# Kernel tuning notes

Hardware: AMD Instinct MI355X
Metric: run time of the kernel (lower is better)

The kernel has to match this reference:

```python
import math
import jax, jax.numpy as jnp
import numpy as np

NUM_BUCKETS = 32
MAX_DISTANCE = 128
N_HEADS = 16
D_KV = 64


def _relative_position_bucket(relative_position, num_buckets=NUM_BUCKETS, max_distance=MAX_DISTANCE):
    # bidirectional (encoder) version, faithful to T5Attention._relative_position_bucket
    nb = num_buckets // 2
    rel_buckets = (relative_position > 0).astype(jnp.int32) * nb
    rp = jnp.abs(relative_position)
    max_exact = nb // 2
    is_small = rp < max_exact
    # log-spaced buckets for large distances; clamp arg of log to >=1 to avoid -inf
    rp_large = max_exact + (
        jnp.log(jnp.maximum(rp, 1).astype(jnp.float32) / max_exact)
        / math.log(max_distance / max_exact)
        * (nb - max_exact)
    ).astype(jnp.int32)
    rp_large = jnp.minimum(rp_large, nb - 1)
    return rel_buckets + jnp.where(is_small, rp, rp_large)


def setup_inputs() -> dict:
    key = jax.random.key(0)
    ks = jax.random.split(key, 6)
    B, S, D = 2, 2048, 1024
    scale = 0.02
    return {
        "hidden_states": jax.random.normal(ks[0], (B, S, D), dtype=jnp.float32),
        "Wq": jax.random.normal(ks[1], (D, N_HEADS * D_KV), dtype=jnp.float32) * scale,
        "Wk": jax.random.normal(ks[2], (D, N_HEADS * D_KV), dtype=jnp.float32) * scale,
        "Wv": jax.random.normal(ks[3], (D, N_HEADS * D_KV), dtype=jnp.float32) * scale,
        "Wo": jax.random.normal(ks[4], (N_HEADS * D_KV, D), dtype=jnp.float32) * scale,
        "rel_bias": jax.random.normal(ks[5], (NUM_BUCKETS, N_HEADS), dtype=jnp.float32),
    }


def reference(hidden_states, Wq, Wk, Wv, Wo, rel_bias):
    B, S, D = hidden_states.shape
    H, dk = N_HEADS, D_KV
    q = (hidden_states @ Wq).reshape(B, S, H, dk)
    k = (hidden_states @ Wk).reshape(B, S, H, dk)
    v = (hidden_states @ Wv).reshape(B, S, H, dk)

    pos = jnp.arange(S)
    relative_position = pos[None, :] - pos[:, None]          # [S_q, S_k]
    buckets = _relative_position_bucket(relative_position)    # [S_q, S_k]
    bias = rel_bias[buckets].transpose(2, 0, 1)               # [H, S_q, S_k]

    # T5 attention: NO 1/sqrt(d) scaling
    scores = jnp.einsum('bqhd,bkhd->bhqk', q, k) + bias[None]
    attn = jax.nn.softmax(scores, axis=-1)
    ctx = jnp.einsum('bhqk,bkhd->bqhd', attn, v).reshape(B, S, H * dk)
    return ctx @ Wo
```

## Files before the change

### kernel.cpp

```cpp
#include <hip/hip_runtime.h>
#include <stdint.h>

#define S_LEN 2048
#define NH 16
#define NB_DELTA (2*S_LEN-1)
#define PST 72

typedef __attribute__((ext_vector_type(8))) __bf16 bf16x8;
typedef __attribute__((ext_vector_type(4))) float f32x4;

__device__ __forceinline__ unsigned short f2bf(float f){
    union { float f; unsigned int u; } v; v.f = f;
    unsigned int u = v.u;
    return (unsigned short)((u + 0x7FFFu + ((u >> 16) & 1u)) >> 16);
}
__device__ __forceinline__ unsigned short f2bf_fast(float f){
    union { float f; unsigned int u; } v; v.f = f;
    return (unsigned short)((v.u + 0x8000u) >> 16);
}
__device__ __forceinline__ float bf2f(unsigned short u){
    union { unsigned int u; float f; } v; v.u = ((unsigned int)u) << 16;
    return v.f;
}

__device__ __forceinline__ void gload16(const void* g, void* l){
    __builtin_amdgcn_global_load_lds(
        (const __attribute__((address_space(1))) void*)(uintptr_t)g,
        (__attribute__((address_space(3))) void*)(uintptr_t)l, 16, 0, 0);
}

__global__ __launch_bounds__(256) void prep_kernel(
    const float* __restrict__ hs, unsigned short* __restrict__ hsb,
    const float* __restrict__ W0, const float* __restrict__ W1,
    const float* __restrict__ W2, const float* __restrict__ W3,
    unsigned short* __restrict__ D0, unsigned short* __restrict__ D1,
    unsigned short* __restrict__ D2, unsigned short* __restrict__ D3,
    const float* __restrict__ rel_bias, float* __restrict__ biasT){
    if (blockIdx.z == 4) {
        int bi = blockIdx.y * 32 + blockIdx.x;
        for (int it = 0; it < 4; it++) {
            int i = bi * 4096 + it * 1024 + threadIdx.x * 4;
            float4 f = *(const float4*)(hs + i);
            ushort4 o;
            o.x = f2bf(f.x); o.y = f2bf(f.y); o.z = f2bf(f.z); o.w = f2bf(f.w);
            *(ushort4*)(hsb + i) = o;
        }
        if (bi < 16) {
            int t = bi * 256 + threadIdx.x;
            if (t < NB_DELTA) {
                int delta = t - (S_LEN - 1);
                int bucket = (delta > 0) ? 16 : 0;
                int a = delta < 0 ? -delta : delta;
                int b;
                if (a < 8) b = a;
                else {
                    int bl = 33 - __builtin_clz(a * a);
                    b = bl < 15 ? bl : 15;
                }
                bucket += b;
                for (int h = 0; h < NH; h++)
                    biasT[h * NB_DELTA + t] = rel_bias[bucket * NH + h];
            }
        }
        return;
    }
    const float* src; unsigned short* dst;
    switch (blockIdx.z) {
        case 0: src = W0; dst = D0; break;
        case 1: src = W1; dst = D1; break;
        case 2: src = W2; dst = D2; break;
        default: src = W3; dst = D3; break;
    }
    __shared__ float tile[32][33];
    int bx = blockIdx.x, by = blockIdx.y;
    int tx = threadIdx.x & 31, ty = threadIdx.x >> 5;
    for (int i = 0; i < 4; i++)
        tile[ty + 8*i][tx] = src[(size_t)(by*32 + ty + 8*i) * 1024 + bx*32 + tx];
    __syncthreads();
    for (int i = 0; i < 4; i++)
        dst[(size_t)(bx*32 + ty + 8*i) * 1024 + by*32 + tx] = f2bf(tile[tx][ty + 8*i]);
}

template<int MODE, int BM>
__global__ __launch_bounds__(256) void gemm_bt_kernel(const unsigned short* __restrict__ A,
                                                      const unsigned short* __restrict__ BT,
                                                      float* __restrict__ C0,
                                                      unsigned short* __restrict__ C1,
                                                      unsigned short* __restrict__ C2,
                                                      int Kdim, int ldc){
    constexpr int IT = BM / 32;
    __shared__ __align__(16) unsigned short As[BM * 32];
    __shared__ __align__(16) unsigned short Bs[128 * 32];
    const int t = threadIdx.x;
    const int wave = t >> 6, lane = t & 63;
    const int quad = lane >> 4, l16 = lane & 15;
    const int wm = (wave >> 1) * (BM / 2), wn = (wave & 1) * 64;
    const size_t row0 = (size_t)blockIdx.y * BM, col0 = (size_t)blockIdx.x * 128;

    const unsigned short* ga = A  + (row0 + wave * (BM/4) + (lane >> 2)) * (size_t)Kdim + (lane & 3) * 8;
    const unsigned short* gb = BT + (col0 + wave * 32 + (lane >> 2)) * (size_t)Kdim + (lane & 3) * 8;
    unsigned short* la0 = &As[(wave * (BM/4)) * 32];
    unsigned short* la1 = &As[(wave * (BM/4) + 16) * 32];
    unsigned short* lb0 = &Bs[(wave * 32) * 32];
    unsigned short* lb1 = &Bs[(wave * 32 + 16) * 32];
    const size_t rstep = (size_t)16 * Kdim;

    f32x4 acc[IT][4] = {};

    for (int kt = 0; kt < Kdim; kt += 32) {
        gload16(ga + kt, la0);
        if (BM == 128) gload16(ga + rstep + kt, la1);
        gload16(gb + kt,         lb0);
        gload16(gb + rstep + kt, lb1);
        __syncthreads();
        bf16x8 a[IT], b[4];
        for (int i = 0; i < IT; i++)
            a[i] = *(const bf16x8*)(&As[(wm + i*16 + l16) * 32 + quad * 8]);
        for (int j = 0; j < 4; j++)
            b[j] = *(const bf16x8*)(&Bs[(wn + j*16 + l16) * 32 + quad * 8]);
        for (int i = 0; i < IT; i++)
            for (int j = 0; j < 4; j++)
                acc[i][j] = __builtin_amdgcn_mfma_f32_16x16x32_bf16(a[i], b[j], acc[i][j], 0, 0, 0);
        __syncthreads();
    }
    for (int i = 0; i < IT; i++)
        for (int j = 0; j < 4; j++) {
            size_t r0 = row0 + wm + i*16 + quad*4;
            size_t c  = col0 + wn + j*16 + l16;
            if (MODE == 0) {
                for (int r = 0; r < 4; r++)
                    C0[(r0 + r) * ldc + c] = acc[i][j][r];
            } else {
                if (c < 2048) {
                    for (int r = 0; r < 4; r++)
                        C1[(r0 + r) * 2048 + c] = f2bf(acc[i][j][r]);
                } else {
                    int bb = (int)(r0 >> 11);
                    int s  = (int)(r0 & 2047);
                    ushort4 pk;
                    pk.x = f2bf(acc[i][j][0]); pk.y = f2bf(acc[i][j][1]);
                    pk.z = f2bf(acc[i][j][2]); pk.w = f2bf(acc[i][j][3]);
                    *(ushort4*)(C2 + ((size_t)(bb * 1024) + (c - 2048)) * 2048 + s) = pk;
                }
            }
        }
}

__global__ __launch_bounds__(256, 4) void flash6_kernel(
    const unsigned short* __restrict__ qk,
    const unsigned short* __restrict__ vt,
    const float* __restrict__ biasT,
    unsigned short* __restrict__ ctxpb,
    float* __restrict__ rsbuf)
{
    const int qt = blockIdx.x, h = blockIdx.y;
    const int b = blockIdx.z >> 1, ck = blockIdx.z & 1;
    const int kt0 = ck << 10;
    const int t = threadIdx.x;
    const int w = t >> 6, lane = t & 63, quad = lane >> 4, l16 = lane & 15;
    const int q0 = qt * 128;

    __shared__ __align__(16) unsigned short KV[4][64 * 32];
    __shared__ __align__(16) unsigned short Pb[128 * PST];
    __shared__ float bias_s[192];

    for (int s = 0; s < 4; s++) {
        int g = t + s * 256;
        int r = g >> 3, c = (g & 7) * 8;
        *(int4*)&Pb[r * PST + c] =
            *(const int4*)(qk + (size_t)(b * S_LEN + q0 + r) * 2048 + h * 64 + c);
    }
    __syncthreads();
    bf16x8 qb[2][2];
    for (int nt = 0; nt < 2; nt++)
        for (int ks = 0; ks < 2; ks++)
            qb[ks][nt] = *(const bf16x8*)&Pb[(w * 32 + nt * 16 + l16) * PST + ks * 32 + quad * 8];

    float rsum[2] = {0.f, 0.f};
    f32x4 ctx[4][2] = {};

    const float* biasRow = biasT + h * NB_DELTA + 2047;

    const int srow = w * 16 + (lane >> 2);
    const int scol = (lane & 3) * 8;
    unsigned short* ldsK0 = &KV[0][w * 16 * 32];
    unsigned short* ldsK1 = &KV[1][w * 16 * 32];
    unsigned short* ldsV0 = &KV[2][w * 16 * 32];
    unsigned short* ldsV1 = &KV[3][w * 16 * 32];

    for (int kt = kt0; kt < kt0 + 1024; kt += 64) {
        __syncthreads();
        {
            const unsigned short* kb = qk + (size_t)(b * S_LEN + kt + srow) * 2048 + 1024 + h * 64 + scol;
            const unsigned short* vb = vt + (size_t)(b * 1024 + h * 64 + srow) * 2048 + kt + scol;
            gload16(kb,      ldsK0);
            gload16(kb + 32, ldsK1);
            gload16(vb,      ldsV0);
            gload16(vb + 32, ldsV1);
            if (t < 192) bias_s[t] = biasRow[kt - q0 - 127 + t] - 16.0f;
        }
        __syncthreads();

        f32x4 st[4][2] = {};
        for (int ks = 0; ks < 2; ks++)
            for (int nb = 0; nb < 4; nb++) {
                bf16x8 ka = *(const bf16x8*)&KV[ks][(nb * 16 + l16) * 32 + quad * 8];
                st[nb][0] = __builtin_amdgcn_mfma_f32_16x16x32_bf16(ka, qb[ks][0], st[nb][0], 0, 0, 0);
                st[nb][1] = __builtin_amdgcn_mfma_f32_16x16x32_bf16(ka, qb[ks][1], st[nb][1], 0, 0, 0);
            }
        for (int nt = 0; nt < 2; nt++) {
            const int ib = quad * 4 + 127 - w * 32 - nt * 16 - l16;
            float rs = 0.f;
            for (int nb = 0; nb < 4; nb++) {
                float e0 = __expf(st[nb][nt][0] + bias_s[ib + nb * 16 + 0]);
                float e1 = __expf(st[nb][nt][1] + bias_s[ib + nb * 16 + 1]);
                float e2 = __expf(st[nb][nt][2] + bias_s[ib + nb * 16 + 2]);
                float e3 = __expf(st[nb][nt][3] + bias_s[ib + nb * 16 + 3]);
                rs += (e0 + e1) + (e2 + e3);
                ushort4 pk;
                pk.x = f2bf_fast(e0); pk.y = f2bf_fast(e1);
                pk.z = f2bf_fast(e2); pk.w = f2bf_fast(e3);
                *(ushort4*)&Pb[(w * 32 + nt * 16 + l16) * PST + nb * 16 + quad * 4] = pk;
            }
            rsum[nt] += rs;
        }
        for (int ks = 0; ks < 2; ks++) {
            bf16x8 pb0 = *(const bf16x8*)&Pb[(w * 32 + l16) * PST + ks * 32 + quad * 8];
            bf16x8 pb1 = *(const bf16x8*)&Pb[(w * 32 + 16 + l16) * PST + ks * 32 + quad * 8];
            for (int nd = 0; nd < 4; nd++) {
                bf16x8 va = *(const bf16x8*)&KV[2 + ks][(nd * 16 + l16) * 32 + quad * 8];
                ctx[nd][0] = __builtin_amdgcn_mfma_f32_16x16x32_bf16(va, pb0, ctx[nd][0], 0, 0, 0);
                ctx[nd][1] = __builtin_amdgcn_mfma_f32_16x16x32_bf16(va, pb1, ctx[nd][1], 0, 0, 0);
            }
        }
    }
    unsigned short* cp = ctxpb + (size_t)ck * 4096 * 1024;
    for (int nt = 0; nt < 2; nt++) {
        float rs = rsum[nt];
        rs += __shfl_xor(rs, 16, 64);
        rs += __shfl_xor(rs, 32, 64);
        int row = b * S_LEN + q0 + w * 32 + nt * 16 + l16;
        if (quad == 0) rsbuf[((size_t)ck * 4096 + row) * 16 + h] = rs;
        for (int nd = 0; nd < 4; nd++) {
            ushort4 pk;
            pk.x = f2bf(ctx[nd][nt][0]); pk.y = f2bf(ctx[nd][nt][1]);
            pk.z = f2bf(ctx[nd][nt][2]); pk.w = f2bf(ctx[nd][nt][3]);
            *(ushort4*)&cp[(size_t)row * 1024 + h * 64 + nd * 16 + quad * 4] = pk;
        }
    }
}

__global__ __launch_bounds__(256) void combine_kernel(const unsigned short* __restrict__ ctxpb,
                                                      const float* __restrict__ rsbuf,
                                                      unsigned short* __restrict__ ctxb){
    int e = blockIdx.x * 256 + threadIdx.x;
    int row = e >> 8;
    int c4 = (e & 255) * 4;
    int h = c4 >> 6;
    float l = rsbuf[(size_t)row * 16 + h] + rsbuf[((size_t)4096 + row) * 16 + h];
    ushort4 a  = *(const ushort4*)&ctxpb[(size_t)row * 1024 + c4];
    ushort4 b2 = *(const ushort4*)&ctxpb[(size_t)4096 * 1024 + (size_t)row * 1024 + c4];
    float inv = 1.f / l;
    ushort4 o;
    o.x = f2bf((bf2f(a.x) + bf2f(b2.x)) * inv);
    o.y = f2bf((bf2f(a.y) + bf2f(b2.y)) * inv);
    o.z = f2bf((bf2f(a.z) + bf2f(b2.z)) * inv);
    o.w = f2bf((bf2f(a.w) + bf2f(b2.w)) * inv);
    *(ushort4*)&ctxb[(size_t)row * 1024 + c4] = o;
}

extern "C" void kernel_launch(void* const* d_in, const int* in_sizes, int n_in,
                              void* d_out, int out_size, void* d_ws, size_t ws_size,
                              hipStream_t stream) {
    const float* hs       = (const float*)d_in[0];
    const float* Wq       = (const float*)d_in[1];
    const float* Wk       = (const float*)d_in[2];
    const float* Wv       = (const float*)d_in[3];
    const float* Wo       = (const float*)d_in[4];
    const float* rel_bias = (const float*)d_in[5];
    float* out = (float*)d_out;

    char* ws = (char*)d_ws;
    float* biasT          = (float*)ws;           ws += 262144;
    unsigned short* hsb   = (unsigned short*)ws;  ws += 8388608;
    unsigned short* WT    = (unsigned short*)ws;  ws += 6291456;
    unsigned short* WoT   = (unsigned short*)ws;  ws += 2097152;
    unsigned short* qkbuf = (unsigned short*)ws;  ws += 16777216;
    unsigned short* Vtg   = (unsigned short*)ws;  ws += 8388608;
    unsigned short* ctxb  = (unsigned short*)ws;  ws += 8388608;
    unsigned short* ctxpb = (unsigned short*)ws;  ws += 16777216;
    float* rsbuf          = (float*)ws;

    prep_kernel<<<dim3(32, 32, 5), 256, 0, stream>>>(
        hs, hsb, Wq, Wk, Wv, Wo,
        WT, WT + 1024 * 1024, WT + 2 * 1024 * 1024, WoT, rel_bias, biasT);

    gemm_bt_kernel<1, 128><<<dim3(24, 32), 256, 0, stream>>>(hsb, WT, nullptr, qkbuf, Vtg, 1024, 0);
    flash6_kernel<<<dim3(S_LEN / 128, NH, 4), 256, 0, stream>>>(qkbuf, Vtg, biasT, ctxpb, rsbuf);
    combine_kernel<<<4096, 256, 0, stream>>>(ctxpb, rsbuf, ctxb);
    gemm_bt_kernel<0, 64><<<dim3(8, 64), 256, 0, stream>>>(ctxb, WoT, out, nullptr, nullptr, 1024, 1024);
}
```

Before: 209.0 us.

## Swizzle LDS tiles with K=64 steps and move V transpose to separate kernel

The GEMM now stages 64-wide K tiles in shared memory with an XOR swizzle, which halves the number of loop iterations and barriers and is meant to avoid LDS bank conflicts. The QKV projection writes a plain row-major [tokens, 3072] buffer instead of a transposed V with strided ushort4 stores, and a new vtrans kernel produces the V^T layout. The flash kernel loads K and V into XOR-swizzled 64x64 LDS tiles. The cost is one extra kernel launch and an extra pass over V through global memory.

New measurement: 207.6 us. Within noise of the previous version (-0.7%).

```diff
diff --git a/kernel.cpp b/kernel.cpp
--- a/kernel.cpp
+++ b/kernel.cpp
@@ -86,41 +86,40 @@
                                                       const unsigned short* __restrict__ BT,
                                                       float* __restrict__ C0,
                                                       unsigned short* __restrict__ C1,
-                                                      unsigned short* __restrict__ C2,
                                                       int Kdim, int ldc){
     constexpr int IT = BM / 32;
-    __shared__ __align__(16) unsigned short As[BM * 32];
-    __shared__ __align__(16) unsigned short Bs[128 * 32];
+    __shared__ __align__(16) unsigned short As[BM * 64];
+    __shared__ __align__(16) unsigned short Bs[128 * 64];
     const int t = threadIdx.x;
     const int wave = t >> 6, lane = t & 63;
     const int quad = lane >> 4, l16 = lane & 15;
     const int wm = (wave >> 1) * (BM / 2), wn = (wave & 1) * 64;
     const size_t row0 = (size_t)blockIdx.y * BM, col0 = (size_t)blockIdx.x * 128;
 
-    const unsigned short* ga = A  + (row0 + wave * (BM/4) + (lane >> 2)) * (size_t)Kdim + (lane & 3) * 8;
-    const unsigned short* gb = BT + (col0 + wave * 32 + (lane >> 2)) * (size_t)Kdim + (lane & 3) * 8;
-    unsigned short* la0 = &As[(wave * (BM/4)) * 32];
-    unsigned short* la1 = &As[(wave * (BM/4) + 16) * 32];
-    unsigned short* lb0 = &Bs[(wave * 32) * 32];
-    unsigned short* lb1 = &Bs[(wave * 32 + 16) * 32];
-    const size_t rstep = (size_t)16 * Kdim;
+    const int srow8 = lane >> 3;
+    const int gg = (lane & 7) ^ srow8;
+    const unsigned short* gA = A  + (row0 + wave * 8 + srow8) * (size_t)Kdim + gg * 8;
+    const unsigned short* gB = BT + (col0 + wave * 8 + srow8) * (size_t)Kdim + gg * 8;
 
     f32x4 acc[IT][4] = {};
 
-    for (int kt = 0; kt < Kdim; kt += 32) {
-        gload16(ga + kt, la0);
-        if (BM == 128) gload16(ga + rstep + kt, la1);
-        gload16(gb + kt,         lb0);
-        gload16(gb + rstep + kt, lb1);
+    for (int kt = 0; kt < Kdim; kt += 64) {
+        for (int p = 0; p < BM / 32; p++)
+            gload16(gA + (size_t)(p * 32) * Kdim + kt, &As[(p * 32 + wave * 8) * 64]);
+        for (int p = 0; p < 4; p++)
+            gload16(gB + (size_t)(p * 32) * Kdim + kt, &Bs[(p * 32 + wave * 8) * 64]);
         __syncthreads();
-        bf16x8 a[IT], b[4];
-        for (int i = 0; i < IT; i++)
-            a[i] = *(const bf16x8*)(&As[(wm + i*16 + l16) * 32 + quad * 8]);
-        for (int j = 0; j < 4; j++)
-            b[j] = *(const bf16x8*)(&Bs[(wn + j*16 + l16) * 32 + quad * 8]);
-        for (int i = 0; i < IT; i++)
+        bf16x8 a[2][IT], b[2][4];
+        for (int ks = 0; ks < 2; ks++) {
+            for (int i = 0; i < IT; i++)
+                a[ks][i] = *(const bf16x8*)(&As[(wm + i*16 + l16) * 64 + (((ks*4 + quad) ^ (l16 & 7)) * 8)]);
             for (int j = 0; j < 4; j++)
-                acc[i][j] = __builtin_amdgcn_mfma_f32_16x16x32_bf16(a[i], b[j], acc[i][j], 0, 0, 0);
+                b[ks][j] = *(const bf16x8*)(&Bs[(wn + j*16 + l16) * 64 + (((ks*4 + quad) ^ (l16 & 7)) * 8)]);
+        }
+        for (int ks = 0; ks < 2; ks++)
+            for (int i = 0; i < IT; i++)
+                for (int j = 0; j < 4; j++)
+                    acc[i][j] = __builtin_amdgcn_mfma_f32_16x16x32_bf16(a[ks][i], b[ks][j], acc[i][j], 0, 0, 0);
         __syncthreads();
     }
     for (int i = 0; i < IT; i++)
@@ -131,23 +130,34 @@
                 for (int r = 0; r < 4; r++)
                     C0[(r0 + r) * ldc + c] = acc[i][j][r];
             } else {
-                if (c < 2048) {
-                    for (int r = 0; r < 4; r++)
-                        C1[(r0 + r) * 2048 + c] = f2bf(acc[i][j][r]);
-                } else {
-                    int bb = (int)(r0 >> 11);
-                    int s  = (int)(r0 & 2047);
-                    ushort4 pk;
-                    pk.x = f2bf(acc[i][j][0]); pk.y = f2bf(acc[i][j][1]);
-                    pk.z = f2bf(acc[i][j][2]); pk.w = f2bf(acc[i][j][3]);
-                    *(ushort4*)(C2 + ((size_t)(bb * 1024) + (c - 2048)) * 2048 + s) = pk;
-                }
-            }
-        }
-}
-
-__global__ __launch_bounds__(256, 4) void flash6_kernel(
-    const unsigned short* __restrict__ qk,
+                for (int r = 0; r < 4; r++)
+                    C1[(r0 + r) * ldc + c] = f2bf(acc[i][j][r]);
+            }
+        }
+}
+
+__global__ __launch_bounds__(256) void vtrans_kernel(const unsigned short* __restrict__ qkv,
+                                                     unsigned short* __restrict__ vt){
+    __shared__ unsigned short tile[64][72];
+    const int v0 = blockIdx.x * 64, s0 = blockIdx.y * 64, b = blockIdx.z;
+    const int tx = threadIdx.x & 7, ty = threadIdx.x >> 3;
+    for (int i = 0; i < 2; i++)
+        *(int4*)&tile[ty + 32*i][tx * 8] =
+            *(const int4*)(qkv + (size_t)(b * 2048 + s0 + ty + 32*i) * 3072 + 2048 + v0 + tx * 8);
+    __syncthreads();
+    for (int i = 0; i < 2; i++) {
+        int v = ty + 32*i;
+        int sl = tx * 8;
+        ushort4 o0, o1;
+        o0.x = tile[sl+0][v]; o0.y = tile[sl+1][v]; o0.z = tile[sl+2][v]; o0.w = tile[sl+3][v];
+        o1.x = tile[sl+4][v]; o1.y = tile[sl+5][v]; o1.z = tile[sl+6][v]; o1.w = tile[sl+7][v];
+        unsigned short* dst = vt + (size_t)(b * 1024 + v0 + v) * 2048 + s0 + sl;
+        *(ushort4*)dst = o0; *(ushort4*)(dst + 4) = o1;
+    }
+}
+
+__global__ __launch_bounds__(256, 4) void flash7_kernel(
+    const unsigned short* __restrict__ qkv,
     const unsigned short* __restrict__ vt,
     const float* __restrict__ biasT,
     unsigned short* __restrict__ ctxpb,
@@ -160,7 +170,8 @@
     const int w = t >> 6, lane = t & 63, quad = lane >> 4, l16 = lane & 15;
     const int q0 = qt * 128;
 
-    __shared__ __align__(16) unsigned short KV[4][64 * 32];
+    __shared__ __align__(16) unsigned short Ks[64 * 64];
+    __shared__ __align__(16) unsigned short Vs[64 * 64];
     __shared__ __align__(16) unsigned short Pb[128 * PST];
     __shared__ float bias_s[192];
 
@@ -168,7 +179,7 @@
         int g = t + s * 256;
         int r = g >> 3, c = (g & 7) * 8;
         *(int4*)&Pb[r * PST + c] =
-            *(const int4*)(qk + (size_t)(b * S_LEN + q0 + r) * 2048 + h * 64 + c);
+            *(const int4*)(qkv + (size_t)(b * S_LEN + q0 + r) * 3072 + h * 64 + c);
     }
     __syncthreads();
     bf16x8 qb[2][2];
@@ -181,22 +192,19 @@
 
     const float* biasRow = biasT + h * NB_DELTA + 2047;
 
-    const int srow = w * 16 + (lane >> 2);
-    const int scol = (lane & 3) * 8;
-    unsigned short* ldsK0 = &KV[0][w * 16 * 32];
-    unsigned short* ldsK1 = &KV[1][w * 16 * 32];
-    unsigned short* ldsV0 = &KV[2][w * 16 * 32];
-    unsigned short* ldsV1 = &KV[3][w * 16 * 32];
+    const int srow8 = lane >> 3;
+    const int gg = (lane & 7) ^ srow8;
+    const int swz = ((l16 & 7) * 8);
 
     for (int kt = kt0; kt < kt0 + 1024; kt += 64) {
         __syncthreads();
         {
-            const unsigned short* kb = qk + (size_t)(b * S_LEN + kt + srow) * 2048 + 1024 + h * 64 + scol;
-            const unsigned short* vb = vt + (size_t)(b * 1024 + h * 64 + srow) * 2048 + kt + scol;
-            gload16(kb,      ldsK0);
-            gload16(kb + 32, ldsK1);
-            gload16(vb,      ldsV0);
-            gload16(vb + 32, ldsV1);
+            const unsigned short* kb = qkv + (size_t)(b * S_LEN + kt + w * 8 + srow8) * 3072 + 1024 + h * 64 + gg * 8;
+            const unsigned short* vb = vt + (size_t)(b * 1024 + h * 64 + w * 8 + srow8) * 2048 + kt + gg * 8;
+            gload16(kb,                         &Ks[(w * 8) * 64]);
+            gload16(kb + (size_t)32 * 3072,     &Ks[(32 + w * 8) * 64]);
+            gload16(vb,                         &Vs[(w * 8) * 64]);
+            gload16(vb + (size_t)32 * 2048,     &Vs[(32 + w * 8) * 64]);
             if (t < 192) bias_s[t] = biasRow[kt - q0 - 127 + t] - 16.0f;
         }
         __syncthreads();
@@ -204,7 +212,7 @@
         f32x4 st[4][2] = {};
         for (int ks = 0; ks < 2; ks++)
             for (int nb = 0; nb < 4; nb++) {
-                bf16x8 ka = *(const bf16x8*)&KV[ks][(nb * 16 + l16) * 32 + quad * 8];
+                bf16x8 ka = *(const bf16x8*)&Ks[(nb * 16 + l16) * 64 + (((ks * 4 + quad) * 8) ^ swz)];
                 st[nb][0] = __builtin_amdgcn_mfma_f32_16x16x32_bf16(ka, qb[ks][0], st[nb][0], 0, 0, 0);
                 st[nb][1] = __builtin_amdgcn_mfma_f32_16x16x32_bf16(ka, qb[ks][1], st[nb][1], 0, 0, 0);
             }
@@ -228,7 +236,7 @@
             bf16x8 pb0 = *(const bf16x8*)&Pb[(w * 32 + l16) * PST + ks * 32 + quad * 8];
             bf16x8 pb1 = *(const bf16x8*)&Pb[(w * 32 + 16 + l16) * PST + ks * 32 + quad * 8];
             for (int nd = 0; nd < 4; nd++) {
-                bf16x8 va = *(const bf16x8*)&KV[2 + ks][(nd * 16 + l16) * 32 + quad * 8];
+                bf16x8 va = *(const bf16x8*)&Vs[(nd * 16 + l16) * 64 + (((ks * 4 + quad) * 8) ^ swz)];
                 ctx[nd][0] = __builtin_amdgcn_mfma_f32_16x16x32_bf16(va, pb0, ctx[nd][0], 0, 0, 0);
                 ctx[nd][1] = __builtin_amdgcn_mfma_f32_16x16x32_bf16(va, pb1, ctx[nd][1], 0, 0, 0);
             }
@@ -285,7 +293,7 @@
     unsigned short* hsb   = (unsigned short*)ws;  ws += 8388608;
     unsigned short* WT    = (unsigned short*)ws;  ws += 6291456;
     unsigned short* WoT   = (unsigned short*)ws;  ws += 2097152;
-    unsigned short* qkbuf = (unsigned short*)ws;  ws += 16777216;
+    unsigned short* qkvb  = (unsigned short*)ws;  ws += 25165824;
     unsigned short* Vtg   = (unsigned short*)ws;  ws += 8388608;
     unsigned short* ctxb  = (unsigned short*)ws;  ws += 8388608;
     unsigned short* ctxpb = (unsigned short*)ws;  ws += 16777216;
@@ -295,8 +303,9 @@
         hs, hsb, Wq, Wk, Wv, Wo,
         WT, WT + 1024 * 1024, WT + 2 * 1024 * 1024, WoT, rel_bias, biasT);
 
-    gemm_bt_kernel<1, 128><<<dim3(24, 32), 256, 0, stream>>>(hsb, WT, nullptr, qkbuf, Vtg, 1024, 0);
-    flash6_kernel<<<dim3(S_LEN / 128, NH, 4), 256, 0, stream>>>(qkbuf, Vtg, biasT, ctxpb, rsbuf);
+    gemm_bt_kernel<1, 128><<<dim3(24, 32), 256, 0, stream>>>(hsb, WT, nullptr, qkvb, 1024, 3072);
+    vtrans_kernel<<<dim3(16, 32, 2), 256, 0, stream>>>(qkvb, Vtg);
+    flash7_kernel<<<dim3(S_LEN / 128, NH, 4), 256, 0, stream>>>(qkvb, Vtg, biasT, ctxpb, rsbuf);
     combine_kernel<<<4096, 256, 0, stream>>>(ctxpb, rsbuf, ctxb);
-    gemm_bt_kernel<0, 64><<<dim3(8, 64), 256, 0, stream>>>(ctxb, WoT, out, nullptr, nullptr, 1024, 1024);
-}
+    gemm_bt_kernel<0, 64><<<dim3(8, 64), 256, 0, stream>>>(ctxb, WoT, out, nullptr, 1024, 1024);
+}
```
